# Kernel tuning notes

Measured on AMD Instinct MI355X. Metric: run time of the kernel, lower is better.

The kernel has to match this reference:

```python
import jax, jax.numpy as jnp
import numpy as np

B, C, H, W = 8, 256, 64, 64   # C = in_channels(64) * no_g(4)
DQK = 8                        # max(in_channels//8, no_g) = max(8,4)


def setup_inputs() -> dict:
    key = jax.random.key(0)
    ks = jax.random.split(key, 8)
    s_in = 1.0 / np.sqrt(C)
    return {
        "x": jax.random.normal(ks[0], (B, C, H, W), dtype=jnp.float32),
        "wq": jax.random.normal(ks[1], (DQK, C), dtype=jnp.float32) * s_in,
        "bq": jax.random.normal(ks[2], (DQK,), dtype=jnp.float32) * 0.01,
        "wk": jax.random.normal(ks[3], (DQK, C), dtype=jnp.float32) * s_in,
        "bk": jax.random.normal(ks[4], (DQK,), dtype=jnp.float32) * 0.01,
        "wv": jax.random.normal(ks[5], (C, C), dtype=jnp.float32) * s_in,
        "bv": jax.random.normal(ks[6], (C,), dtype=jnp.float32) * 0.01,
        "gamma": jax.random.normal(ks[7], (1,), dtype=jnp.float32) * 0.5,
    }


def reference(x, wq, bq, wk, bk, wv, bv, gamma):
    b, c, h, w = x.shape
    n = h * w
    xf = x.reshape(b, c, n)                                   # B,C,N
    q = (jnp.einsum('bcn,qc->bqn', xf, wq) + bq[None, :, None])  # B,DQK,N (1x1 conv)
    k = (jnp.einsum('bcn,qc->bqn', xf, wk) + bk[None, :, None])  # B,DQK,N
    v = (jnp.einsum('bcn,oc->bon', xf, wv) + bv[None, :, None])  # B,C,N
    energy = jnp.einsum('bdn,bdm->bnm', q, k)                 # B,N,N (no scale, as in source)
    attn = jax.nn.softmax(energy, axis=-1)                    # softmax over last dim
    # out[b,c,m] = sum_n v[b,c,n] * attn[b,m,n]  (bmm(V, A^T))
    out = jnp.einsum('bcn,bmn->bcm', v, attn).reshape(b, c, h, w)
    return gamma[0] * out + x
```

## Files before the change

### kernel.cpp

```cpp
#include <hip/hip_runtime.h>
#include <math.h>

namespace {

constexpr int B_ = 8;
constexpr int C_ = 256;
constexpr int N_ = 4096;

constexpr int TM = 64;
constexpr int TN = 128;
constexpr int NCH = N_ / TN;
constexpr int PSTRIDE = 136;
constexpr float LOG2E = 1.4426950408889634f;

constexpr int VBLK = C_ * 16;

typedef __attribute__((ext_vector_type(8))) short short8;
typedef __attribute__((ext_vector_type(16))) float float16;

__device__ inline unsigned short f2bf(float f) {
  unsigned u = __float_as_uint(f);
  u += 0x7FFFu + ((u >> 16) & 1u);
  return (unsigned short)(u >> 16);
}
__device__ inline float bf2f(unsigned short h) {
  return __uint_as_float(((unsigned)h) << 16);
}

__device__ inline float fast_exp2(float x) {
  float r;
  asm("v_exp_f32 %0, %1" : "=v"(r) : "v"(x));
  return r;
}

__global__ __launch_bounds__(256) void prep_kernel(
    const float* __restrict__ wv, const float* __restrict__ wq,
    const float* __restrict__ wk,
    unsigned short* __restrict__ wv_bf, unsigned short* __restrict__ wqk_bf) {
  const int i = blockIdx.x * 256 + threadIdx.x;
  wv_bf[i] = f2bf(wv[i]);
  if (i < 2048) {
    const int d = i >> 8, c = i & 255;
    const float qL = wq[i] * LOG2E;
    const unsigned short hq = f2bf(qL);
    wqk_bf[d * 256 + c]        = hq;
    wqk_bf[(d + 8) * 256 + c]  = f2bf(qL - bf2f(hq));
    const float kv = wk[i];
    const unsigned short hk = f2bf(kv);
    wqk_bf[(d + 16) * 256 + c] = hk;
    wqk_bf[(d + 24) * 256 + c] = f2bf(kv - bf2f(hk));
  }
}

__device__ inline short8 xfrag(const float* xs, int c0, int n) {
  const float* base = xs + c0 * 32 + n;
  uint4 p;
  asm("v_cvt_pk_bf16_f32 %0, %1, %2" : "=v"(p.x) : "v"(base[0]),   "v"(base[32]));
  asm("v_cvt_pk_bf16_f32 %0, %1, %2" : "=v"(p.y) : "v"(base[64]),  "v"(base[96]));
  asm("v_cvt_pk_bf16_f32 %0, %1, %2" : "=v"(p.z) : "v"(base[128]), "v"(base[160]));
  asm("v_cvt_pk_bf16_f32 %0, %1, %2" : "=v"(p.w) : "v"(base[192]), "v"(base[224]));
  return __builtin_bit_cast(short8, p);
}

__global__ __launch_bounds__(256, 4) void proj_kernel(
    const float* __restrict__ x,
    const float* __restrict__ bq, const float* __restrict__ bk,
    const unsigned short* __restrict__ wqk_bf,
    const unsigned short* __restrict__ wv_bf, const float* __restrict__ bv,
    unsigned short* __restrict__ q_t, unsigned short* __restrict__ k_th,
    unsigned short* __restrict__ k_tl, unsigned short* __restrict__ v)
{
  __shared__ float xs[256 * 32];

  const int b = blockIdx.y;
  const int n0 = blockIdx.x * 32;
  const int tid = threadIdx.x;
  const int w = tid >> 6, l = tid & 63;
  const int l31 = l & 31, lh = l >> 5;

  {
    const int r8 = l >> 3, c4 = (l & 7) * 4;
    const float* gp = x + ((size_t)b * C_ + w * 64 + r8) * N_ + n0 + c4;
    #pragma unroll
    for (int i = 0; i < 64; i += 8) {
      __builtin_amdgcn_global_load_lds(
          (const __attribute__((address_space(1))) void*)(gp + (size_t)i * N_),
          (__attribute__((address_space(3))) void*)(xs + (w * 64 + i) * 32), 16, 0, 0);
    }
  }
  __syncthreads();

  if (w == 0) {
    float16 sacc;
    #pragma unroll
    for (int r = 0; r < 16; ++r) sacc[r] = 0.f;
    for (int ks = 0; ks < 16; ++ks) {
      const short8 a = *reinterpret_cast<const short8*>(
          wqk_bf + l31 * 256 + ks * 16 + lh * 8);
      const short8 bfg = xfrag(xs, ks * 16 + lh * 8, l31);
      sacc = __builtin_amdgcn_mfma_f32_32x32x16_bf16(a, bfg, sacc, 0, 0, 0);
    }
    const size_t gn = (size_t)b * N_ + n0 + l31;
    #pragma unroll
    for (int r = 0; r < 4; ++r) {
      const int d = r + 4 * lh;
      const float qv = sacc[r] + sacc[r + 4] + bq[d] * LOG2E;
      const unsigned short hq = f2bf(qv);
      q_t[gn * 16 + d]     = hq;
      q_t[gn * 16 + 8 + d] = f2bf(qv - bf2f(hq));
      const float kv = sacc[r + 8] + sacc[r + 12] + bk[d];
      const unsigned short hk = f2bf(kv);
      k_th[gn * 8 + d] = hk;
      k_tl[gn * 8 + d] = f2bf(kv - bf2f(hk));
    }
  }

  float16 acc[2];
  #pragma unroll
  for (int mi = 0; mi < 2; ++mi)
    #pragma unroll
    for (int r = 0; r < 16; ++r) acc[mi][r] = 0.f;

  for (int ks = 0; ks < 16; ++ks) {
    short8 af[2];
    #pragma unroll
    for (int mi = 0; mi < 2; ++mi)
      af[mi] = *reinterpret_cast<const short8*>(
          wv_bf + (w * 64 + mi * 32 + l31) * C_ + ks * 16 + lh * 8);
    const short8 bfg = xfrag(xs, ks * 16 + lh * 8, l31);
    #pragma unroll
    for (int mi = 0; mi < 2; ++mi)
      acc[mi] = __builtin_amdgcn_mfma_f32_32x32x16_bf16(af[mi], bfg, acc[mi], 0, 0, 0);
  }

  const int p32 = (l31 & 3) | (((l31 >> 3) & 3) << 2) | (((l31 >> 2) & 1) << 4);
  const int P32 = n0 + p32;
  const int nblk = P32 >> 4, nin = P32 & 15;
  #pragma unroll
  for (int mi = 0; mi < 2; ++mi)
    #pragma unroll
    for (int r = 0; r < 16; ++r) {
      const int c = w * 64 + mi * 32 + (r & 3) + 8 * (r >> 2) + 4 * lh;
      v[(((size_t)b * (N_ / 16) + nblk) * C_ + c) * 16 + nin] =
          f2bf(acc[mi][r] + bv[c]);
    }
}

__global__ __launch_bounds__(512, 4) void attn_kernel(
    const unsigned short* __restrict__ q_t, const unsigned short* __restrict__ k_th,
    const unsigned short* __restrict__ k_tl, const unsigned short* __restrict__ v,
    const float* __restrict__ x, const float* __restrict__ gamma,
    float* __restrict__ out)
{
  __shared__ __align__(16) unsigned short ps[2][TM][PSTRIDE];
  __shared__ float rsp[4][TM];
  __shared__ float rsn[TM];

  const int b = blockIdx.x;
  const int m0 = blockIdx.y * TM;
  const int tid = threadIdx.x;
  const int w = tid >> 6;
  const int l = tid & 63;
  const int l31 = l & 31, lh = l >> 5;
  const int mt = w >> 2, nt = w & 3;
  const int nrow = nt * 32 + l31;
  const int mcol = 32 * mt + l31;

  const size_t qoff = ((size_t)b * N_ + m0 + mcol) * 16;
  const short8 qh = *reinterpret_cast<const short8*>(q_t + qoff);
  const short8 ql = *reinterpret_cast<const short8*>(q_t + qoff + 8);

  const unsigned short* kb = (lh ? k_tl : k_th) + (size_t)b * N_ * 8;

  const unsigned short* vlane =
      v + ((size_t)b * (N_ / 16)) * VBLK + (size_t)(w * 32 + l31) * 16 + lh * 8;

  float16 o0, o1;
  #pragma unroll
  for (int r = 0; r < 16; ++r) { o0[r] = 0.f; o1[r] = 0.f; }
  float rsum = 0.f;

  short8 af[8];
  #pragma unroll
  for (int g = 0; g < 8; ++g)
    af[g] = *reinterpret_cast<const short8*>(vlane + (size_t)g * VBLK);
  short8 kf1 = *reinterpret_cast<const short8*>(kb + (size_t)(TN + nrow) * 8);
  {
    const short8 kf0 = *reinterpret_cast<const short8*>(kb + (size_t)nrow * 8);
    float16 s;
    #pragma unroll
    for (int r = 0; r < 16; ++r) s[r] = 0.f;
    s = __builtin_amdgcn_mfma_f32_32x32x16_bf16(kf0, qh, s, 0, 0, 0);
    s = __builtin_amdgcn_mfma_f32_32x32x16_bf16(kf0, ql, s, 0, 0, 0);
    float e[16];
    #pragma unroll
    for (int r = 0; r < 16; ++r) e[r] = fast_exp2(s[r]);
    rsum += (((e[0] + e[1]) + (e[2] + e[3])) + ((e[4] + e[5]) + (e[6] + e[7]))) +
            (((e[8] + e[9]) + (e[10] + e[11])) + ((e[12] + e[13]) + (e[14] + e[15])));
    uint4 pk0, pk1;
    asm("v_cvt_pk_bf16_f32 %0, %1, %2" : "=v"(pk0.x) : "v"(e[0]), "v"(e[1]));
    asm("v_cvt_pk_bf16_f32 %0, %1, %2" : "=v"(pk0.y) : "v"(e[2]), "v"(e[3]));
    asm("v_cvt_pk_bf16_f32 %0, %1, %2" : "=v"(pk0.z) : "v"(e[4]), "v"(e[5]));
    asm("v_cvt_pk_bf16_f32 %0, %1, %2" : "=v"(pk0.w) : "v"(e[6]), "v"(e[7]));
    asm("v_cvt_pk_bf16_f32 %0, %1, %2" : "=v"(pk1.x) : "v"(e[8]), "v"(e[9]));
    asm("v_cvt_pk_bf16_f32 %0, %1, %2" : "=v"(pk1.y) : "v"(e[10]), "v"(e[11]));
    asm("v_cvt_pk_bf16_f32 %0, %1, %2" : "=v"(pk1.z) : "v"(e[12]), "v"(e[13]));
    asm("v_cvt_pk_bf16_f32 %0, %1, %2" : "=v"(pk1.w) : "v"(e[14]), "v"(e[15]));
    unsigned short* prow = &ps[0][mcol][nt * 32 + lh * 16];
    *reinterpret_cast<uint4*>(prow) = pk0;
    *reinterpret_cast<uint4*>(prow + 8) = pk1;
  }
  __syncthreads();

  #pragma unroll 2
  for (int nc = 0; nc < NCH; ++nc) {
    const int buf = nc & 1;
    const bool more = (nc + 1) < NCH;
    const int nc1 = more ? (nc + 1) : 0;
    const int n2 = ((nc + 2) < NCH ? (nc + 2) : 0) * TN;

    const short8 kf2 = *reinterpret_cast<const short8*>(kb + (size_t)(n2 + nrow) * 8);

    if (more) {
      float16 s;
      #pragma unroll
      for (int r = 0; r < 16; ++r) s[r] = 0.f;
      s = __builtin_amdgcn_mfma_f32_32x32x16_bf16(kf1, qh, s, 0, 0, 0);
      s = __builtin_amdgcn_mfma_f32_32x32x16_bf16(kf1, ql, s, 0, 0, 0);
      float e[16];
      #pragma unroll
      for (int r = 0; r < 16; ++r) e[r] = fast_exp2(s[r]);
      rsum += (((e[0] + e[1]) + (e[2] + e[3])) + ((e[4] + e[5]) + (e[6] + e[7]))) +
              (((e[8] + e[9]) + (e[10] + e[11])) + ((e[12] + e[13]) + (e[14] + e[15])));
      uint4 pk0, pk1;
      asm("v_cvt_pk_bf16_f32 %0, %1, %2" : "=v"(pk0.x) : "v"(e[0]), "v"(e[1]));
      asm("v_cvt_pk_bf16_f32 %0, %1, %2" : "=v"(pk0.y) : "v"(e[2]), "v"(e[3]));
      asm("v_cvt_pk_bf16_f32 %0, %1, %2" : "=v"(pk0.z) : "v"(e[4]), "v"(e[5]));
      asm("v_cvt_pk_bf16_f32 %0, %1, %2" : "=v"(pk0.w) : "v"(e[6]), "v"(e[7]));
      asm("v_cvt_pk_bf16_f32 %0, %1, %2" : "=v"(pk1.x) : "v"(e[8]), "v"(e[9]));
      asm("v_cvt_pk_bf16_f32 %0, %1, %2" : "=v"(pk1.y) : "v"(e[10]), "v"(e[11]));
      asm("v_cvt_pk_bf16_f32 %0, %1, %2" : "=v"(pk1.z) : "v"(e[12]), "v"(e[13]));
      asm("v_cvt_pk_bf16_f32 %0, %1, %2" : "=v"(pk1.w) : "v"(e[14]), "v"(e[15]));
      unsigned short* prow = &ps[buf ^ 1][mcol][nt * 32 + lh * 16];
      *reinterpret_cast<uint4*>(prow) = pk0;
      *reinterpret_cast<uint4*>(prow + 8) = pk1;
    }

    __builtin_amdgcn_s_setprio(1);
    #pragma unroll
    for (int ks = 0; ks < 8; ++ks) {
      const short8 p0 = *reinterpret_cast<const short8*>(&ps[buf][l31][ks * 16 + lh * 8]);
      const short8 p1 = *reinterpret_cast<const short8*>(&ps[buf][32 + l31][ks * 16 + lh * 8]);
      o0 = __builtin_amdgcn_mfma_f32_32x32x16_bf16(af[ks], p0, o0, 0, 0, 0);
      o1 = __builtin_amdgcn_mfma_f32_32x32x16_bf16(af[ks], p1, o1, 0, 0, 0);
      af[ks] = *reinterpret_cast<const short8*>(vlane + (size_t)(nc1 * 8 + ks) * VBLK);
    }
    __builtin_amdgcn_s_setprio(0);

    kf1 = kf2;
    __syncthreads();
  }

  rsum += __shfl_xor(rsum, 32);
  if (l < 32) rsp[nt][mcol] = rsum;
  __syncthreads();
  if (tid < TM) rsn[tid] = rsp[0][tid] + rsp[1][tid] + rsp[2][tid] + rsp[3][tid];
  __syncthreads();

  const float g = gamma[0];
  const float t0 = g / rsn[l31];
  const float t1 = g / rsn[32 + l31];
  #pragma unroll
  for (int r = 0; r < 16; ++r) {
    const int c = 32 * w + (r & 3) + 8 * (r >> 2) + 4 * lh;
    const size_t i0 = ((size_t)b * C_ + c) * N_ + m0 + l31;
    out[i0]      = fmaf(o0[r], t0, x[i0]);
    out[i0 + 32] = fmaf(o1[r], t1, x[i0 + 32]);
  }
}

}

extern "C" void kernel_launch(void* const* d_in, const int* in_sizes, int n_in,
                              void* d_out, int out_size, void* d_ws, size_t ws_size,
                              hipStream_t stream) {
  const float* x     = (const float*)d_in[0];
  const float* wq    = (const float*)d_in[1];
  const float* bq    = (const float*)d_in[2];
  const float* wk    = (const float*)d_in[3];
  const float* bk    = (const float*)d_in[4];
  const float* wv    = (const float*)d_in[5];
  const float* bv    = (const float*)d_in[6];
  const float* gamma = (const float*)d_in[7];
  float* out = (float*)d_out;

  char* p = (char*)d_ws;
  unsigned short* q_t    = (unsigned short*)p;  p += (size_t)B_ * N_ * 16 * 2;
  unsigned short* k_th   = (unsigned short*)p;  p += (size_t)B_ * N_ * 8 * 2;
  unsigned short* k_tl   = (unsigned short*)p;  p += (size_t)B_ * N_ * 8 * 2;
  unsigned short* wv_bf  = (unsigned short*)p;  p += (size_t)C_ * C_ * 2;
  unsigned short* wqk_bf = (unsigned short*)p;  p += (size_t)32 * C_ * 2;
  unsigned short* v      = (unsigned short*)p;

  prep_kernel<<<dim3(C_ * C_ / 256), 256, 0, stream>>>(wv, wq, wk, wv_bf, wqk_bf);
  proj_kernel<<<dim3(N_ / 32, B_), 256, 0, stream>>>(x, bq, bk, wqk_bf, wv_bf, bv,
                                                     q_t, k_th, k_tl, v);
  attn_kernel<<<dim3(B_, N_ / TM), 512, 0, stream>>>(q_t, k_th, k_tl, v, x, gamma, out);
}
```

Measured before the change: 197.3 us.

## Halve attention block to 4 warps, each computing two channel and query tiles

The attention kernel now launches 256 threads (4 waves) per block instead of 512. Each wave computes the QK^T/exp tile for both 32-row query halves and accumulates two 32-channel slices of the output (four accumulators), so each P fragment read from LDS feeds twice as many MFMAs. The aim is fewer LDS reads and less per-wave sync overhead per unit of MFMA work. In exchange, register pressure roughly doubles (af0/af1, four float16 accumulators), occupancy hints drop to (256,2), and the unroll-2 pragma is removed, which may cut latency hiding.

```diff
diff --git a/kernel.cpp b/kernel.cpp
--- a/kernel.cpp
+++ b/kernel.cpp
@@ -146,7 +146,7 @@
     }
 }
 
-__global__ __launch_bounds__(512, 4) void attn_kernel(
+__global__ __launch_bounds__(256, 2) void attn_kernel(
     const unsigned short* __restrict__ q_t, const unsigned short* __restrict__ k_th,
     const unsigned short* __restrict__ k_tl, const unsigned short* __restrict__ v,
     const float* __restrict__ x, const float* __restrict__ gamma,
@@ -162,41 +162,37 @@
   const int w = tid >> 6;
   const int l = tid & 63;
   const int l31 = l & 31, lh = l >> 5;
-  const int mt = w >> 2, nt = w & 3;
-  const int nrow = nt * 32 + l31;
-  const int mcol = 32 * mt + l31;
-
-  const size_t qoff = ((size_t)b * N_ + m0 + mcol) * 16;
-  const short8 qh = *reinterpret_cast<const short8*>(q_t + qoff);
-  const short8 ql = *reinterpret_cast<const short8*>(q_t + qoff + 8);
+  const int nrow = w * 32 + l31;
+
+  const size_t qoff0 = ((size_t)b * N_ + m0 + l31) * 16;
+  const short8 qh0 = *reinterpret_cast<const short8*>(q_t + qoff0);
+  const short8 ql0 = *reinterpret_cast<const short8*>(q_t + qoff0 + 8);
+  const short8 qh1 = *reinterpret_cast<const short8*>(q_t + qoff0 + 512);
+  const short8 ql1 = *reinterpret_cast<const short8*>(q_t + qoff0 + 520);
 
   const unsigned short* kb = (lh ? k_tl : k_th) + (size_t)b * N_ * 8;
 
-  const unsigned short* vlane =
-      v + ((size_t)b * (N_ / 16)) * VBLK + (size_t)(w * 32 + l31) * 16 + lh * 8;
-
-  float16 o0, o1;
-  #pragma unroll
-  for (int r = 0; r < 16; ++r) { o0[r] = 0.f; o1[r] = 0.f; }
-  float rsum = 0.f;
-
-  short8 af[8];
-  #pragma unroll
-  for (int g = 0; g < 8; ++g)
-    af[g] = *reinterpret_cast<const short8*>(vlane + (size_t)g * VBLK);
-  short8 kf1 = *reinterpret_cast<const short8*>(kb + (size_t)(TN + nrow) * 8);
-  {
-    const short8 kf0 = *reinterpret_cast<const short8*>(kb + (size_t)nrow * 8);
+  const unsigned short* vlane0 =
+      v + ((size_t)b * (N_ / 16)) * VBLK + (size_t)(2 * w * 32 + l31) * 16 + lh * 8;
+  const unsigned short* vlane1 = vlane0 + 512;
+
+  float16 o00, o01, o10, o11;
+  #pragma unroll
+  for (int r = 0; r < 16; ++r) { o00[r] = 0.f; o01[r] = 0.f; o10[r] = 0.f; o11[r] = 0.f; }
+  float rsum0 = 0.f, rsum1 = 0.f;
+
+  auto qk_tile = [&](const short8& kf, const short8& qh, const short8& ql,
+                     float& rs, unsigned short* prow) {
     float16 s;
     #pragma unroll
     for (int r = 0; r < 16; ++r) s[r] = 0.f;
-    s = __builtin_amdgcn_mfma_f32_32x32x16_bf16(kf0, qh, s, 0, 0, 0);
-    s = __builtin_amdgcn_mfma_f32_32x32x16_bf16(kf0, ql, s, 0, 0, 0);
+    s = __builtin_amdgcn_mfma_f32_32x32x16_bf16(kf, qh, s, 0, 0, 0);
+    s = __builtin_amdgcn_mfma_f32_32x32x16_bf16(kf, ql, s, 0, 0, 0);
     float e[16];
     #pragma unroll
     for (int r = 0; r < 16; ++r) e[r] = fast_exp2(s[r]);
-    rsum += (((e[0] + e[1]) + (e[2] + e[3])) + ((e[4] + e[5]) + (e[6] + e[7]))) +
-            (((e[8] + e[9]) + (e[10] + e[11])) + ((e[12] + e[13]) + (e[14] + e[15])));
+    rs += (((e[0] + e[1]) + (e[2] + e[3])) + ((e[4] + e[5]) + (e[6] + e[7]))) +
+          (((e[8] + e[9]) + (e[10] + e[11])) + ((e[12] + e[13]) + (e[14] + e[15])));
     uint4 pk0, pk1;
     asm("v_cvt_pk_bf16_f32 %0, %1, %2" : "=v"(pk0.x) : "v"(e[0]), "v"(e[1]));
     asm("v_cvt_pk_bf16_f32 %0, %1, %2" : "=v"(pk0.y) : "v"(e[2]), "v"(e[3]));
@@ -206,13 +202,24 @@
     asm("v_cvt_pk_bf16_f32 %0, %1, %2" : "=v"(pk1.y) : "v"(e[10]), "v"(e[11]));
     asm("v_cvt_pk_bf16_f32 %0, %1, %2" : "=v"(pk1.z) : "v"(e[12]), "v"(e[13]));
     asm("v_cvt_pk_bf16_f32 %0, %1, %2" : "=v"(pk1.w) : "v"(e[14]), "v"(e[15]));
-    unsigned short* prow = &ps[0][mcol][nt * 32 + lh * 16];
     *reinterpret_cast<uint4*>(prow) = pk0;
     *reinterpret_cast<uint4*>(prow + 8) = pk1;
+  };
+
+  short8 af0[8], af1[8];
+  #pragma unroll
+  for (int g = 0; g < 8; ++g) {
+    af0[g] = *reinterpret_cast<const short8*>(vlane0 + (size_t)g * VBLK);
+    af1[g] = *reinterpret_cast<const short8*>(vlane1 + (size_t)g * VBLK);
+  }
+  short8 kf1 = *reinterpret_cast<const short8*>(kb + (size_t)(TN + nrow) * 8);
+  {
+    const short8 kf0 = *reinterpret_cast<const short8*>(kb + (size_t)nrow * 8);
+    qk_tile(kf0, qh0, ql0, rsum0, &ps[0][l31][w * 32 + lh * 16]);
+    qk_tile(kf0, qh1, ql1, rsum1, &ps[0][32 + l31][w * 32 + lh * 16]);
   }
   __syncthreads();
 
-  #pragma unroll 2
   for (int nc = 0; nc < NCH; ++nc) {
     const int buf = nc & 1;
     const bool more = (nc + 1) < NCH;
@@ -222,28 +229,8 @@
     const short8 kf2 = *reinterpret_cast<const short8*>(kb + (size_t)(n2 + nrow) * 8);
 
     if (more) {
-      float16 s;
-      #pragma unroll
-      for (int r = 0; r < 16; ++r) s[r] = 0.f;
-      s = __builtin_amdgcn_mfma_f32_32x32x16_bf16(kf1, qh, s, 0, 0, 0);
-      s = __builtin_amdgcn_mfma_f32_32x32x16_bf16(kf1, ql, s, 0, 0, 0);
-      float e[16];
-      #pragma unroll
-      for (int r = 0; r < 16; ++r) e[r] = fast_exp2(s[r]);
-      rsum += (((e[0] + e[1]) + (e[2] + e[3])) + ((e[4] + e[5]) + (e[6] + e[7]))) +
-              (((e[8] + e[9]) + (e[10] + e[11])) + ((e[12] + e[13]) + (e[14] + e[15])));
-      uint4 pk0, pk1;
-      asm("v_cvt_pk_bf16_f32 %0, %1, %2" : "=v"(pk0.x) : "v"(e[0]), "v"(e[1]));
-      asm("v_cvt_pk_bf16_f32 %0, %1, %2" : "=v"(pk0.y) : "v"(e[2]), "v"(e[3]));
-      asm("v_cvt_pk_bf16_f32 %0, %1, %2" : "=v"(pk0.z) : "v"(e[4]), "v"(e[5]));
-      asm("v_cvt_pk_bf16_f32 %0, %1, %2" : "=v"(pk0.w) : "v"(e[6]), "v"(e[7]));
-      asm("v_cvt_pk_bf16_f32 %0, %1, %2" : "=v"(pk1.x) : "v"(e[8]), "v"(e[9]));
-      asm("v_cvt_pk_bf16_f32 %0, %1, %2" : "=v"(pk1.y) : "v"(e[10]), "v"(e[11]));
-      asm("v_cvt_pk_bf16_f32 %0, %1, %2" : "=v"(pk1.z) : "v"(e[12]), "v"(e[13]));
-      asm("v_cvt_pk_bf16_f32 %0, %1, %2" : "=v"(pk1.w) : "v"(e[14]), "v"(e[15]));
-      unsigned short* prow = &ps[buf ^ 1][mcol][nt * 32 + lh * 16];
-      *reinterpret_cast<uint4*>(prow) = pk0;
-      *reinterpret_cast<uint4*>(prow + 8) = pk1;
+      qk_tile(kf1, qh0, ql0, rsum0, &ps[buf ^ 1][l31][w * 32 + lh * 16]);
+      qk_tile(kf1, qh1, ql1, rsum1, &ps[buf ^ 1][32 + l31][w * 32 + lh * 16]);
     }
 
     __builtin_amdgcn_s_setprio(1);
@@ -251,9 +238,12 @@
     for (int ks = 0; ks < 8; ++ks) {
       const short8 p0 = *reinterpret_cast<const short8*>(&ps[buf][l31][ks * 16 + lh * 8]);
       const short8 p1 = *reinterpret_cast<const short8*>(&ps[buf][32 + l31][ks * 16 + lh * 8]);
-      o0 = __builtin_amdgcn_mfma_f32_32x32x16_bf16(af[ks], p0, o0, 0, 0, 0);
-      o1 = __builtin_amdgcn_mfma_f32_32x32x16_bf16(af[ks], p1, o1, 0, 0, 0);
-      af[ks] = *reinterpret_cast<const short8*>(vlane + (size_t)(nc1 * 8 + ks) * VBLK);
+      o00 = __builtin_amdgcn_mfma_f32_32x32x16_bf16(af0[ks], p0, o00, 0, 0, 0);
+      o01 = __builtin_amdgcn_mfma_f32_32x32x16_bf16(af0[ks], p1, o01, 0, 0, 0);
+      o10 = __builtin_amdgcn_mfma_f32_32x32x16_bf16(af1[ks], p0, o10, 0, 0, 0);
+      o11 = __builtin_amdgcn_mfma_f32_32x32x16_bf16(af1[ks], p1, o11, 0, 0, 0);
+      af0[ks] = *reinterpret_cast<const short8*>(vlane0 + (size_t)(nc1 * 8 + ks) * VBLK);
+      af1[ks] = *reinterpret_cast<const short8*>(vlane1 + (size_t)(nc1 * 8 + ks) * VBLK);
     }
     __builtin_amdgcn_s_setprio(0);
 
@@ -261,8 +251,9 @@
     __syncthreads();
   }
 
-  rsum += __shfl_xor(rsum, 32);
-  if (l < 32) rsp[nt][mcol] = rsum;
+  rsum0 += __shfl_xor(rsum0, 32);
+  rsum1 += __shfl_xor(rsum1, 32);
+  if (l < 32) { rsp[w][l31] = rsum0; rsp[w][32 + l31] = rsum1; }
   __syncthreads();
   if (tid < TM) rsn[tid] = rsp[0][tid] + rsp[1][tid] + rsp[2][tid] + rsp[3][tid];
   __syncthreads();
@@ -272,10 +263,14 @@
   const float t1 = g / rsn[32 + l31];
   #pragma unroll
   for (int r = 0; r < 16; ++r) {
-    const int c = 32 * w + (r & 3) + 8 * (r >> 2) + 4 * lh;
-    const size_t i0 = ((size_t)b * C_ + c) * N_ + m0 + l31;
-    out[i0]      = fmaf(o0[r], t0, x[i0]);
-    out[i0 + 32] = fmaf(o1[r], t1, x[i0 + 32]);
+    const int crow = (r & 3) + 8 * (r >> 2) + 4 * lh;
+    const int c0 = 2 * w * 32 + crow;
+    const size_t i00 = ((size_t)b * C_ + c0) * N_ + m0 + l31;
+    const size_t i10 = i00 + (size_t)32 * N_;
+    out[i00]      = fmaf(o00[r], t0, x[i00]);
+    out[i00 + 32] = fmaf(o01[r], t1, x[i00 + 32]);
+    out[i10]      = fmaf(o10[r], t0, x[i10]);
+    out[i10 + 32] = fmaf(o11[r], t1, x[i10 + 32]);
   }
 }
 
@@ -305,5 +300,5 @@
   prep_kernel<<<dim3(C_ * C_ / 256), 256, 0, stream>>>(wv, wq, wk, wv_bf, wqk_bf);
   proj_kernel<<<dim3(N_ / 32, B_), 256, 0, stream>>>(x, bq, bk, wqk_bf, wv_bf, bv,
                                                      q_t, k_th, k_tl, v);
-  attn_kernel<<<dim3(B_, N_ / TM), 512, 0, stream>>>(q_t, k_th, k_tl, v, x, gamma, out);
-}
+  attn_kernel<<<dim3(B_, N_ / TM), 256, 0, stream>>>(q_t, k_th, k_tl, v, x, gamma, out);
+}
```

Result: faster. 192.0 us (-2.7%).
